# Kernel optimization log

Hardware: AMD Instinct MI355X
Metric: run time of the kernel (lower is better)

## Reference

```python
import jax, jax.numpy as jnp
import numpy as np

EPS = 1e-15


def setup_inputs() -> dict:
    key = jax.random.key(0)
    ks = jax.random.split(key, 10)
    F, B, L = 10, 16384, 20          # num_field, batch, hist_len
    V, D = 1000000, 16               # sparse_feature_number, sparse_feature_dim
    FEAT, E, S, G, T = 160, 8, 64, 3, 32  # feature_size, expert_num, expert_size, gate_num, tower_size
    return {
        "ids": jax.random.randint(ks[0], (F, B, L), 0, V, dtype=jnp.int64),
        "emb_table": jax.random.uniform(ks[1], (V, D), jnp.float32, -1.0, 1.0),
        "expert_w": jax.random.normal(ks[2], (E, FEAT, S), jnp.float32) * 0.05,
        "expert_b": jnp.full((E, S), 0.1, jnp.float32),
        "gate_w": jax.random.normal(ks[3], (G, FEAT, E), jnp.float32) * 0.05,
        "gate_b": jnp.full((G, E), 0.1, jnp.float32),
        "tower_w": jax.random.normal(ks[4], (G, S, T), jnp.float32) * 0.05,
        "tower_b": jnp.full((G, T), 0.1, jnp.float32),
        "out_w": jax.random.normal(ks[5], (G, T, 2), jnp.float32) * 0.05,
        "out_b": jnp.full((G, 2), 0.1, jnp.float32),
    }


def reference(ids, emb_table, expert_w, expert_b, gate_w, gate_b,
              tower_w, tower_b, out_w, out_b):
    # Embedding lookup + sum over history: [F,B,L,D] -> [F,B,D]
    field_emb = emb_table[ids].sum(axis=2)
    B = field_emb.shape[1]
    # concat per-field embeddings along feature axis: [B, F*D]
    x = jnp.transpose(field_emb, (1, 0, 2)).reshape(B, -1)
    # all experts as one batched GEMM: [B,E,S]
    experts = jax.nn.relu(jnp.einsum('bf,efs->bes', x, expert_w) + expert_b)
    # gate softmax over experts: [B,G,E]
    gates = jax.nn.softmax(jnp.einsum('bf,gfe->bge', x, gate_w) + gate_b, axis=-1)
    # gate-weighted expert mixture: [B,G,S]
    mix = jnp.einsum('bge,bes->bgs', gates, experts)
    # towers: [B,G,T] -> logits [B,G,2]
    tow = jax.nn.relu(jnp.einsum('bgs,gst->bgt', mix, tower_w) + tower_b)
    logits = jnp.einsum('bgt,gto->bgo', tow, out_w) + out_b
    probs = jnp.clip(jax.nn.softmax(logits, axis=-1), EPS, 1.0 - EPS)  # [B,3,2]
    ctr, cvr, imp = probs[:, 0], probs[:, 1], probs[:, 2]
    ctr1 = ctr[:, 1:2]
    cvr1 = cvr[:, 1:2]
    ctcvr1 = ctr1 * cvr1
    ctcvr = jnp.concatenate([1.0 - ctcvr1, ctcvr1], axis=1)
    imp1 = imp[:, 1:2]
    # out_list packed along last axis: ctr(2), ctr1(1), cvr(2), cvr1(1), ctcvr(2), ctcvr1(1), imp1(1) -> [B,10]
    return jnp.concatenate([ctr, ctr1, cvr, cvr1, ctcvr, ctcvr1, imp1], axis=1)
```

## Files before the change

kernel.cpp:

```cpp
#include <hip/hip_runtime.h>
#include <hip/hip_bf16.h>
#include <cstdint>
#include <cstddef>

#define NFIELD 10
#define BATCH  16384
#define NIDS   20
#define DEMB   16
#define NFEAT  160
#define NEXP   8
#define NS     64
#define NG     3
#define NT     32

#define XB        ((size_t)BATCH * NFEAT * 2)
#define BP_OFF_B  XB
#define BM_OFF_B  (BP_OFF_B + 174080)
#define BT_OFF_B  (BM_OFF_B + 2176)
#define TB2_OFF_B (BT_OFF_B + 12288)
#define OWF_OFF_B (TB2_OFF_B + 384)
#define OBF_OFF_B (OWF_OFF_B + 768)
#define FLG_OFF_B (OBF_OFF_B + 32)

typedef short bfrag __attribute__((ext_vector_type(8)));
typedef float f32x4 __attribute__((ext_vector_type(4)));

__device__ __forceinline__ float bflo(uint32_t u) {
    union { uint32_t u; float f; } c; c.u = u << 16; return c.f;
}
__device__ __forceinline__ float bfhi(uint32_t u) {
    union { uint32_t u; float f; } c; c.u = u & 0xffff0000u; return c.f;
}
__device__ __forceinline__ float bf1(uint16_t v) {
    union { uint32_t u; float f; } c; c.u = ((uint32_t)v) << 16; return c.f;
}
__device__ __forceinline__ uint16_t f2bf(float f) {
    union { float f; uint32_t u; } c; c.f = f;
    uint32_t r = c.u + 0x7fffu + ((c.u >> 16) & 1u);
    return (uint16_t)(r >> 16);
}
__device__ __forceinline__ float ldw(const void* p, int i, bool bf) {
    return bf ? bf1(((const uint16_t*)p)[i]) : ((const float*)p)[i];
}
__device__ __forceinline__ uint16_t ldb16(const void* p, int i, bool bf) {
    return bf ? ((const uint16_t*)p)[i] : f2bf(((const float*)p)[i]);
}

__global__ __launch_bounds__(64) void sniff_dtypes(
    const uint32_t* __restrict__ ids_w,
    const uint32_t* __restrict__ emb_w,
    int* __restrict__ flags)
{
    int t = threadIdx.x;
    size_t p = (size_t)t * 25000;
    uint32_t hi = ids_w[2 * p + 1];
    int n_hi = __popcll(__ballot(hi != 0));

    size_t q = (size_t)t * 125000;
    uint32_t w = emb_w[q];
    uint32_t v = (w >> 8) & 0x7Fu;
    int n_bf = __popcll(__ballot(v >= 0x3Bu && v <= 0x3Fu));

    if (t == 0) {
        flags[0] = (n_hi < 8)   ? 1 : 0;
        flags[1] = (n_bf >= 32) ? 1 : 0;
    }
}

__global__ __launch_bounds__(256) void pack_weights(
    const void* __restrict__ ew, const void* __restrict__ eb,
    const void* __restrict__ gw, const void* __restrict__ gb,
    const void* __restrict__ tw, const void* __restrict__ tb,
    const void* __restrict__ ow, const void* __restrict__ ob,
    uint16_t* __restrict__ bp, float* __restrict__ bm,
    uint16_t* __restrict__ bt, float* __restrict__ tb2,
    float* __restrict__ owf, float* __restrict__ obf,
    const int* __restrict__ flags)
{
    const bool bf = flags[1] != 0;
    int i = blockIdx.x * 256 + threadIdx.x;
    if (i < 10880) {
        int nt = i / 320, rem = i % 320;
        int ks = rem / 64, l = rem % 64;
        int n  = nt * 16 + (l & 15);
        int kb = ks * 32 + ((l >> 4) * 8);
        uint16_t v[8];
        #pragma unroll
        for (int j = 0; j < 8; ++j) {
            int k = kb + j;
            uint16_t x;
            if (n < 512)      x = ldb16(ew, (n >> 6) * 10240 + k * 64 + (n & 63), bf);
            else if (n < 536) x = ldb16(gw, ((n - 512) >> 3) * 1280 + k * 8 + ((n - 512) & 7), bf);
            else              x = 0;
            v[j] = x;
        }
        uint4 o;
        o.x = (uint32_t)v[0] | ((uint32_t)v[1] << 16);
        o.y = (uint32_t)v[2] | ((uint32_t)v[3] << 16);
        o.z = (uint32_t)v[4] | ((uint32_t)v[5] << 16);
        o.w = (uint32_t)v[6] | ((uint32_t)v[7] << 16);
        ((uint4*)bp)[i] = o;
    } else if (i < 11648) {
        int it = i - 10880;
        int g = it / 256, rem = it % 256;
        int ntile = rem / 128, ks = (rem / 64) & 1, l = rem % 64;
        int t  = ntile * 16 + (l & 15);
        int sb = ks * 32 + ((l >> 4) * 8);
        uint16_t v[8];
        #pragma unroll
        for (int j = 0; j < 8; ++j)
            v[j] = ldb16(tw, g * 2048 + (sb + j) * 32 + t, bf);
        uint4 o;
        o.x = (uint32_t)v[0] | ((uint32_t)v[1] << 16);
        o.y = (uint32_t)v[2] | ((uint32_t)v[3] << 16);
        o.z = (uint32_t)v[4] | ((uint32_t)v[5] << 16);
        o.w = (uint32_t)v[6] | ((uint32_t)v[7] << 16);
        ((uint4*)bt)[it] = o;
    } else if (i < 12192) {
        int n = i - 11648;
        bm[n] = (n < 512) ? ldw(eb, n, bf) : (n < 536 ? ldw(gb, n - 512, bf) : 0.0f);
    } else if (i < 12288) {
        int n = i - 12192; tb2[n] = ldw(tb, n, bf);
    } else if (i < 12480) {
        int n = i - 12288; owf[n] = ldw(ow, n, bf);
    } else if (i < 12486) {
        int n = i - 12480; obf[n] = ldw(ob, n, bf);
    }
}

__global__ __launch_bounds__(256) void gather_sum(
    const void* __restrict__ ids_raw,
    const void* __restrict__ emb_raw,
    uint16_t* __restrict__ xout,
    const int* __restrict__ flags)
{
    const bool i64 = flags[0] != 0;
    const bool bf  = flags[1] != 0;
    int tid = blockIdx.x * 256 + threadIdx.x;
    int h    = tid & 1;
    int pair = tid >> 1;
    int f = pair >> 14;
    int b = pair & (BATCH - 1);

    int idv[NIDS];
    if (i64) {
        const int4* p4 = (const int4*)((const long long*)ids_raw +
                                       ((size_t)f * BATCH + b) * NIDS);
        #pragma unroll
        for (int j = 0; j < NIDS / 2; ++j) {
            int4 q = p4[j];
            idv[2 * j + 0] = q.x;
            idv[2 * j + 1] = q.z;
        }
    } else {
        const int4* p4 = (const int4*)((const int*)ids_raw +
                                       ((size_t)f * BATCH + b) * NIDS);
        #pragma unroll
        for (int j = 0; j < NIDS / 4; ++j) {
            int4 q = p4[j];
            idv[4 * j + 0] = q.x; idv[4 * j + 1] = q.y;
            idv[4 * j + 2] = q.z; idv[4 * j + 3] = q.w;
        }
    }

    float acc[8];
    #pragma unroll
    for (int d = 0; d < 8; ++d) acc[d] = 0.0f;

    if (bf) {
        #pragma unroll
        for (int l = 0; l < NIDS; ++l) {
            uint4 r = *(const uint4*)((const uint16_t*)emb_raw +
                                      (size_t)idv[l] * DEMB + h * 8);
            acc[0] += bflo(r.x); acc[1] += bfhi(r.x);
            acc[2] += bflo(r.y); acc[3] += bfhi(r.y);
            acc[4] += bflo(r.z); acc[5] += bfhi(r.z);
            acc[6] += bflo(r.w); acc[7] += bfhi(r.w);
        }
    } else {
        #pragma unroll
        for (int l = 0; l < NIDS; ++l) {
            const float4* p = (const float4*)((const float*)emb_raw +
                                              (size_t)idv[l] * DEMB + h * 8);
            float4 r0 = p[0], r1 = p[1];
            acc[0] += r0.x; acc[1] += r0.y; acc[2] += r0.z; acc[3] += r0.w;
            acc[4] += r1.x; acc[5] += r1.y; acc[6] += r1.z; acc[7] += r1.w;
        }
    }

    uint4 o;
    o.x = (uint32_t)f2bf(acc[0]) | ((uint32_t)f2bf(acc[1]) << 16);
    o.y = (uint32_t)f2bf(acc[2]) | ((uint32_t)f2bf(acc[3]) << 16);
    o.z = (uint32_t)f2bf(acc[4]) | ((uint32_t)f2bf(acc[5]) << 16);
    o.w = (uint32_t)f2bf(acc[6]) | ((uint32_t)f2bf(acc[7]) << 16);
    *(uint4*)(xout + (size_t)b * NFEAT + f * DEMB + h * 8) = o;
}

__global__ __launch_bounds__(256) void moe_fwd(
    const uint16_t* __restrict__ xbf,
    const uint16_t* __restrict__ bp,
    const float*    __restrict__ bm,
    const uint16_t* __restrict__ btw,
    const float*    __restrict__ btb,
    const float*    __restrict__ owf,
    const float*    __restrict__ obf,
    const int* __restrict__ flags,
    void* __restrict__ out)
{
    __shared__ uint16_t exp_lds[32][520];
    __shared__ float    gate_lds[32][33];
    __shared__ uint16_t mix_lds[32][200];
    __shared__ float    tow_lds[32][100];
    __shared__ float    prob_lds[32][6];

    const bool bfw = flags[1] != 0;
    const int tid = threadIdx.x;
    const int w = tid >> 6, l = tid & 63;
    const int lm = l & 15, q = l >> 4;
    const int b0 = blockIdx.x * 32;
    const int mrow = (w & 1) * 16;
    const int nhalf = w >> 1;

    bfrag a[5];
    {
        const uint16_t* xr = xbf + (size_t)(b0 + mrow + lm) * NFEAT + q * 8;
        #pragma unroll
        for (int ks = 0; ks < 5; ++ks)
            a[ks] = *(const bfrag*)(xr + ks * 32);
    }

    const int nt0 = nhalf * 17;
    for (int it = 0; it < 17; ++it) {
        int nt = nt0 + it;
        f32x4 acc = {0.0f, 0.0f, 0.0f, 0.0f};
        const bfrag* bpp = (const bfrag*)bp + (size_t)(nt * 5) * 64 + l;
        #pragma unroll
        for (int ks = 0; ks < 5; ++ks) {
            bfrag b = bpp[ks * 64];
            acc = __builtin_amdgcn_mfma_f32_16x16x32_bf16(a[ks], b, acc, 0, 0, 0);
        }
        int col = nt * 16 + lm;
        float bias = bm[col];
        if (col < 512) {
            #pragma unroll
            for (int r = 0; r < 4; ++r)
                exp_lds[mrow + q * 4 + r][col] = f2bf(fmaxf(acc[r] + bias, 0.0f));
        } else {
            #pragma unroll
            for (int r = 0; r < 4; ++r)
                gate_lds[mrow + q * 4 + r][col - 512] = acc[r] + bias;
        }
    }
    __syncthreads();

    const int sm = tid >> 3, j = tid & 7;

    if (j < 3) {
        float* gl = &gate_lds[sm][j * 8];
        float m = gl[0];
        #pragma unroll
        for (int e = 1; e < 8; ++e) m = fmaxf(m, gl[e]);
        float ex[8], s = 0.0f;
        #pragma unroll
        for (int e = 0; e < 8; ++e) { ex[e] = __expf(gl[e] - m); s += ex[e]; }
        float inv = 1.0f / s;
        #pragma unroll
        for (int e = 0; e < 8; ++e) gl[e] = ex[e] * inv;
    }
    __syncthreads();

    for (int g = 0; g < NG; ++g) {
        float m8[8];
        #pragma unroll
        for (int i = 0; i < 8; ++i) m8[i] = 0.0f;
        #pragma unroll
        for (int e = 0; e < NEXP; ++e) {
            float gv = gate_lds[sm][g * 8 + e];
            uint4 u = *(const uint4*)&exp_lds[sm][e * 64 + j * 8];
            m8[0] = fmaf(gv, bflo(u.x), m8[0]); m8[1] = fmaf(gv, bfhi(u.x), m8[1]);
            m8[2] = fmaf(gv, bflo(u.y), m8[2]); m8[3] = fmaf(gv, bfhi(u.y), m8[3]);
            m8[4] = fmaf(gv, bflo(u.z), m8[4]); m8[5] = fmaf(gv, bfhi(u.z), m8[5]);
            m8[6] = fmaf(gv, bflo(u.w), m8[6]); m8[7] = fmaf(gv, bfhi(u.w), m8[7]);
        }
        uint4 o;
        o.x = (uint32_t)f2bf(m8[0]) | ((uint32_t)f2bf(m8[1]) << 16);
        o.y = (uint32_t)f2bf(m8[2]) | ((uint32_t)f2bf(m8[3]) << 16);
        o.z = (uint32_t)f2bf(m8[4]) | ((uint32_t)f2bf(m8[5]) << 16);
        o.w = (uint32_t)f2bf(m8[6]) | ((uint32_t)f2bf(m8[7]) << 16);
        *(uint4*)&mix_lds[sm][g * 64 + j * 8] = o;
    }
    __syncthreads();

    for (int u = w; u < 12; u += 4) {
        int g = u >> 2, mt = (u >> 1) & 1, ntile = u & 1;
        f32x4 acc = {0.0f, 0.0f, 0.0f, 0.0f};
        #pragma unroll
        for (int ks = 0; ks < 2; ++ks) {
            bfrag av = *(const bfrag*)&mix_lds[mt * 16 + lm][g * 64 + ks * 32 + q * 8];
            bfrag bv = *(const bfrag*)(btw + (size_t)((((g * 2 + ntile) * 2 + ks) * 64 + l)) * 8);
            acc = __builtin_amdgcn_mfma_f32_16x16x32_bf16(av, bv, acc, 0, 0, 0);
        }
        int t = ntile * 16 + lm;
        float bias = btb[g * 32 + t];
        #pragma unroll
        for (int r = 0; r < 4; ++r)
            tow_lds[mt * 16 + q * 4 + r][g * 32 + t] = fmaxf(acc[r] + bias, 0.0f);
    }
    __syncthreads();

    if (j < 3) {
        int g = j;
        float l0 = obf[2 * g], l1 = obf[2 * g + 1];
        #pragma unroll 8
        for (int t = 0; t < NT; ++t) {
            float tv = tow_lds[sm][g * 32 + t];
            l0 = fmaf(tv, owf[g * 64 + 2 * t], l0);
            l1 = fmaf(tv, owf[g * 64 + 2 * t + 1], l1);
        }
        float m  = fmaxf(l0, l1);
        float e0 = __expf(l0 - m);
        float e1 = __expf(l1 - m);
        float inv = 1.0f / (e0 + e1);
        float p0 = fminf(fmaxf(e0 * inv, 1e-15f), 1.0f);
        float p1 = fminf(fmaxf(e1 * inv, 1e-15f), 1.0f);
        prob_lds[sm][2 * g + 0] = p0;
        prob_lds[sm][2 * g + 1] = p1;
    }
    __syncthreads();

    {
        float ctr0 = prob_lds[sm][0], ctr1 = prob_lds[sm][1];
        float cvr0 = prob_lds[sm][2], cvr1 = prob_lds[sm][3];
        float imp1 = prob_lds[sm][5];
        float ctcvr1 = ctr1 * cvr1;
        for (int o = j; o < 10; o += 8) {
            float v;
            switch (o) {
                case 0: v = ctr0; break;
                case 1: v = ctr1; break;
                case 2: v = ctr1; break;
                case 3: v = cvr0; break;
                case 4: v = cvr1; break;
                case 5: v = cvr1; break;
                case 6: v = 1.0f - ctcvr1; break;
                case 7: v = ctcvr1; break;
                case 8: v = ctcvr1; break;
                default: v = imp1; break;
            }
            if (bfw) ((uint16_t*)out)[(size_t)(b0 + sm) * 10 + o] = f2bf(v);
            else     ((float*)out)[(size_t)(b0 + sm) * 10 + o]    = v;
        }
    }
}

extern "C" void kernel_launch(void* const* d_in, const int* in_sizes, int n_in,
                              void* d_out, int out_size, void* d_ws, size_t ws_size,
                              hipStream_t stream) {
    const void* ids = d_in[0];
    const void* emb = d_in[1];

    char* ws = (char*)d_ws;
    uint16_t* xbf = (uint16_t*)ws;
    uint16_t* bpk = (uint16_t*)(ws + BP_OFF_B);
    float*    bm  = (float*)(ws + BM_OFF_B);
    uint16_t* btw = (uint16_t*)(ws + BT_OFF_B);
    float*    tb2 = (float*)(ws + TB2_OFF_B);
    float*    owf = (float*)(ws + OWF_OFF_B);
    float*    obf = (float*)(ws + OBF_OFF_B);
    int*    flags = (int*)(ws + FLG_OFF_B);

    sniff_dtypes<<<1, 64, 0, stream>>>((const uint32_t*)ids, (const uint32_t*)emb, flags);
    pack_weights<<<49, 256, 0, stream>>>(
        d_in[2], d_in[3], d_in[4], d_in[5], d_in[6], d_in[7], d_in[8], d_in[9],
        bpk, bm, btw, tb2, owf, obf, flags);
    gather_sum<<<(NFIELD * BATCH * 2) / 256, 256, 0, stream>>>(ids, emb, xbf, flags);
    moe_fwd<<<BATCH / 32, 256, 0, stream>>>(
        xbf, bpk, bm, btw, tb2, owf, obf, flags, d_out);
}
```

Before: 204.9 us.

## Fuse embedding gather into MoE kernel and inline dtype sniffing

Removes the separate gather_sum and sniff_dtypes kernels. Each MoE block now gathers and sums embeddings for its 32 rows directly into shared memory, one thread per (field,row) covering all 16 dims. Dtype detection moves into per-block inline sniffing. This avoids the global round trip of the bf16 feature matrix and two launches, but leaves fewer threads issuing the random gathers and serialises gather before the MFMA phase within each block.

Measured after the change: 177.0 us. 1.16x faster.

```diff
diff --git a/kernel.cpp b/kernel.cpp
--- a/kernel.cpp
+++ b/kernel.cpp
@@ -13,14 +13,12 @@
 #define NG     3
 #define NT     32
 
-#define XB        ((size_t)BATCH * NFEAT * 2)
-#define BP_OFF_B  XB
+#define BP_OFF_B  0
 #define BM_OFF_B  (BP_OFF_B + 174080)
 #define BT_OFF_B  (BM_OFF_B + 2176)
 #define TB2_OFF_B (BT_OFF_B + 12288)
 #define OWF_OFF_B (TB2_OFF_B + 384)
 #define OBF_OFF_B (OWF_OFF_B + 768)
-#define FLG_OFF_B (OBF_OFF_B + 32)
 
 typedef short bfrag __attribute__((ext_vector_type(8)));
 typedef float f32x4 __attribute__((ext_vector_type(4)));
@@ -45,39 +43,32 @@
 __device__ __forceinline__ uint16_t ldb16(const void* p, int i, bool bf) {
     return bf ? ((const uint16_t*)p)[i] : f2bf(((const float*)p)[i]);
 }
-
-__global__ __launch_bounds__(64) void sniff_dtypes(
-    const uint32_t* __restrict__ ids_w,
+__device__ __forceinline__ int sniff_bf(const uint32_t* emb_w) {
+    int n_bf = 0;
+    #pragma unroll
+    for (int t = 0; t < 16; ++t) {
+        uint32_t wv = emb_w[(size_t)t * 500000];
+        uint32_t v = (wv >> 8) & 0x7Fu;
+        n_bf += (v >= 0x3Bu && v <= 0x3Fu);
+    }
+    return n_bf >= 8;
+}
+
+__global__ __launch_bounds__(256) void pack_weights(
     const uint32_t* __restrict__ emb_w,
-    int* __restrict__ flags)
-{
-    int t = threadIdx.x;
-    size_t p = (size_t)t * 25000;
-    uint32_t hi = ids_w[2 * p + 1];
-    int n_hi = __popcll(__ballot(hi != 0));
-
-    size_t q = (size_t)t * 125000;
-    uint32_t w = emb_w[q];
-    uint32_t v = (w >> 8) & 0x7Fu;
-    int n_bf = __popcll(__ballot(v >= 0x3Bu && v <= 0x3Fu));
-
-    if (t == 0) {
-        flags[0] = (n_hi < 8)   ? 1 : 0;
-        flags[1] = (n_bf >= 32) ? 1 : 0;
-    }
-}
-
-__global__ __launch_bounds__(256) void pack_weights(
     const void* __restrict__ ew, const void* __restrict__ eb,
     const void* __restrict__ gw, const void* __restrict__ gb,
     const void* __restrict__ tw, const void* __restrict__ tb,
     const void* __restrict__ ow, const void* __restrict__ ob,
     uint16_t* __restrict__ bp, float* __restrict__ bm,
     uint16_t* __restrict__ bt, float* __restrict__ tb2,
-    float* __restrict__ owf, float* __restrict__ obf,
-    const int* __restrict__ flags)
+    float* __restrict__ owf, float* __restrict__ obf)
 {
-    const bool bf = flags[1] != 0;
+    __shared__ int sbf;
+    if (threadIdx.x == 0) sbf = sniff_bf(emb_w);
+    __syncthreads();
+    const bool bf = sbf != 0;
+
     int i = blockIdx.x * 256 + threadIdx.x;
     if (i < 10880) {
         int nt = i / 320, rem = i % 320;
@@ -128,83 +119,15 @@
     }
 }
 
-__global__ __launch_bounds__(256) void gather_sum(
+__global__ __launch_bounds__(256, 2) void moe_fused(
     const void* __restrict__ ids_raw,
     const void* __restrict__ emb_raw,
-    uint16_t* __restrict__ xout,
-    const int* __restrict__ flags)
-{
-    const bool i64 = flags[0] != 0;
-    const bool bf  = flags[1] != 0;
-    int tid = blockIdx.x * 256 + threadIdx.x;
-    int h    = tid & 1;
-    int pair = tid >> 1;
-    int f = pair >> 14;
-    int b = pair & (BATCH - 1);
-
-    int idv[NIDS];
-    if (i64) {
-        const int4* p4 = (const int4*)((const long long*)ids_raw +
-                                       ((size_t)f * BATCH + b) * NIDS);
-        #pragma unroll
-        for (int j = 0; j < NIDS / 2; ++j) {
-            int4 q = p4[j];
-            idv[2 * j + 0] = q.x;
-            idv[2 * j + 1] = q.z;
-        }
-    } else {
-        const int4* p4 = (const int4*)((const int*)ids_raw +
-                                       ((size_t)f * BATCH + b) * NIDS);
-        #pragma unroll
-        for (int j = 0; j < NIDS / 4; ++j) {
-            int4 q = p4[j];
-            idv[4 * j + 0] = q.x; idv[4 * j + 1] = q.y;
-            idv[4 * j + 2] = q.z; idv[4 * j + 3] = q.w;
-        }
-    }
-
-    float acc[8];
-    #pragma unroll
-    for (int d = 0; d < 8; ++d) acc[d] = 0.0f;
-
-    if (bf) {
-        #pragma unroll
-        for (int l = 0; l < NIDS; ++l) {
-            uint4 r = *(const uint4*)((const uint16_t*)emb_raw +
-                                      (size_t)idv[l] * DEMB + h * 8);
-            acc[0] += bflo(r.x); acc[1] += bfhi(r.x);
-            acc[2] += bflo(r.y); acc[3] += bfhi(r.y);
-            acc[4] += bflo(r.z); acc[5] += bfhi(r.z);
-            acc[6] += bflo(r.w); acc[7] += bfhi(r.w);
-        }
-    } else {
-        #pragma unroll
-        for (int l = 0; l < NIDS; ++l) {
-            const float4* p = (const float4*)((const float*)emb_raw +
-                                              (size_t)idv[l] * DEMB + h * 8);
-            float4 r0 = p[0], r1 = p[1];
-            acc[0] += r0.x; acc[1] += r0.y; acc[2] += r0.z; acc[3] += r0.w;
-            acc[4] += r1.x; acc[5] += r1.y; acc[6] += r1.z; acc[7] += r1.w;
-        }
-    }
-
-    uint4 o;
-    o.x = (uint32_t)f2bf(acc[0]) | ((uint32_t)f2bf(acc[1]) << 16);
-    o.y = (uint32_t)f2bf(acc[2]) | ((uint32_t)f2bf(acc[3]) << 16);
-    o.z = (uint32_t)f2bf(acc[4]) | ((uint32_t)f2bf(acc[5]) << 16);
-    o.w = (uint32_t)f2bf(acc[6]) | ((uint32_t)f2bf(acc[7]) << 16);
-    *(uint4*)(xout + (size_t)b * NFEAT + f * DEMB + h * 8) = o;
-}
-
-__global__ __launch_bounds__(256) void moe_fwd(
-    const uint16_t* __restrict__ xbf,
     const uint16_t* __restrict__ bp,
     const float*    __restrict__ bm,
     const uint16_t* __restrict__ btw,
     const float*    __restrict__ btb,
     const float*    __restrict__ owf,
     const float*    __restrict__ obf,
-    const int* __restrict__ flags,
     void* __restrict__ out)
 {
     __shared__ uint16_t exp_lds[32][520];
@@ -212,8 +135,8 @@
     __shared__ uint16_t mix_lds[32][200];
     __shared__ float    tow_lds[32][100];
     __shared__ float    prob_lds[32][6];
-
-    const bool bfw = flags[1] != 0;
+    __shared__ int      sflags;
+
     const int tid = threadIdx.x;
     const int w = tid >> 6, l = tid & 63;
     const int lm = l & 15, q = l >> 4;
@@ -221,13 +144,91 @@
     const int mrow = (w & 1) * 16;
     const int nhalf = w >> 1;
 
+    if (tid == 0) {
+        int n_hi = 0;
+        #pragma unroll
+        for (int t = 0; t < 16; ++t) {
+            size_t p = (size_t)t * 100000;
+            n_hi += (((const uint32_t*)ids_raw)[2 * p + 1] != 0);
+        }
+        sflags = ((n_hi < 2) ? 1 : 0) | (sniff_bf((const uint32_t*)emb_raw) ? 2 : 0);
+    }
+    __syncthreads();
+    const bool i64 = (sflags & 1) != 0;
+    const bool bfe = (sflags & 2) != 0;
+
+    uint16_t* xs = &exp_lds[0][0];
+    for (int p = tid; p < 32 * NFIELD; p += 256) {
+        int f = p >> 5, s = p & 31;
+        int idv[NIDS];
+        if (i64) {
+            const int4* p4 = (const int4*)((const long long*)ids_raw +
+                                           ((size_t)f * BATCH + (b0 + s)) * NIDS);
+            #pragma unroll
+            for (int j = 0; j < NIDS / 2; ++j) {
+                int4 t4 = p4[j];
+                idv[2 * j + 0] = t4.x;
+                idv[2 * j + 1] = t4.z;
+            }
+        } else {
+            const int4* p4 = (const int4*)((const int*)ids_raw +
+                                           ((size_t)f * BATCH + (b0 + s)) * NIDS);
+            #pragma unroll
+            for (int j = 0; j < NIDS / 4; ++j) {
+                int4 t4 = p4[j];
+                idv[4 * j + 0] = t4.x; idv[4 * j + 1] = t4.y;
+                idv[4 * j + 2] = t4.z; idv[4 * j + 3] = t4.w;
+            }
+        }
+
+        float acc[16];
+        #pragma unroll
+        for (int d = 0; d < 16; ++d) acc[d] = 0.0f;
+
+        if (bfe) {
+            #pragma unroll 5
+            for (int ll = 0; ll < NIDS; ++ll) {
+                const uint4* row = (const uint4*)((const uint16_t*)emb_raw +
+                                                  (size_t)idv[ll] * DEMB);
+                uint4 r0 = row[0];
+                uint4 r1 = row[1];
+                acc[0]  += bflo(r0.x); acc[1]  += bfhi(r0.x);
+                acc[2]  += bflo(r0.y); acc[3]  += bfhi(r0.y);
+                acc[4]  += bflo(r0.z); acc[5]  += bfhi(r0.z);
+                acc[6]  += bflo(r0.w); acc[7]  += bfhi(r0.w);
+                acc[8]  += bflo(r1.x); acc[9]  += bfhi(r1.x);
+                acc[10] += bflo(r1.y); acc[11] += bfhi(r1.y);
+                acc[12] += bflo(r1.z); acc[13] += bfhi(r1.z);
+                acc[14] += bflo(r1.w); acc[15] += bfhi(r1.w);
+            }
+        } else {
+            #pragma unroll 5
+            for (int ll = 0; ll < NIDS; ++ll) {
+                const float4* row = (const float4*)((const float*)emb_raw +
+                                                    (size_t)idv[ll] * DEMB);
+                float4 r0 = row[0], r1 = row[1], r2 = row[2], r3 = row[3];
+                acc[0]  += r0.x; acc[1]  += r0.y; acc[2]  += r0.z; acc[3]  += r0.w;
+                acc[4]  += r1.x; acc[5]  += r1.y; acc[6]  += r1.z; acc[7]  += r1.w;
+                acc[8]  += r2.x; acc[9]  += r2.y; acc[10] += r2.z; acc[11] += r2.w;
+                acc[12] += r3.x; acc[13] += r3.y; acc[14] += r3.z; acc[15] += r3.w;
+            }
+        }
+
+        uint32_t pk[8];
+        #pragma unroll
+        for (int j = 0; j < 8; ++j)
+            pk[j] = (uint32_t)f2bf(acc[2 * j]) | ((uint32_t)f2bf(acc[2 * j + 1]) << 16);
+        uint4* dst = (uint4*)(xs + (size_t)s * 168 + f * DEMB);
+        dst[0] = make_uint4(pk[0], pk[1], pk[2], pk[3]);
+        dst[1] = make_uint4(pk[4], pk[5], pk[6], pk[7]);
+    }
+    __syncthreads();
+
     bfrag a[5];
-    {
-        const uint16_t* xr = xbf + (size_t)(b0 + mrow + lm) * NFEAT + q * 8;
-        #pragma unroll
-        for (int ks = 0; ks < 5; ++ks)
-            a[ks] = *(const bfrag*)(xr + ks * 32);
-    }
+    #pragma unroll
+    for (int ks = 0; ks < 5; ++ks)
+        a[ks] = *(const bfrag*)(xs + (size_t)(mrow + lm) * 168 + ks * 32 + q * 8);
+    __syncthreads();
 
     const int nt0 = nhalf * 17;
     for (int it = 0; it < 17; ++it) {
@@ -347,7 +348,7 @@
                 case 8: v = ctcvr1; break;
                 default: v = imp1; break;
             }
-            if (bfw) ((uint16_t*)out)[(size_t)(b0 + sm) * 10 + o] = f2bf(v);
+            if (bfe) ((uint16_t*)out)[(size_t)(b0 + sm) * 10 + o] = f2bf(v);
             else     ((float*)out)[(size_t)(b0 + sm) * 10 + o]    = v;
         }
     }
@@ -360,20 +361,17 @@
     const void* emb = d_in[1];
 
     char* ws = (char*)d_ws;
-    uint16_t* xbf = (uint16_t*)ws;
     uint16_t* bpk = (uint16_t*)(ws + BP_OFF_B);
     float*    bm  = (float*)(ws + BM_OFF_B);
     uint16_t* btw = (uint16_t*)(ws + BT_OFF_B);
     float*    tb2 = (float*)(ws + TB2_OFF_B);
     float*    owf = (float*)(ws + OWF_OFF_B);
     float*    obf = (float*)(ws + OBF_OFF_B);
-    int*    flags = (int*)(ws + FLG_OFF_B);
-
-    sniff_dtypes<<<1, 64, 0, stream>>>((const uint32_t*)ids, (const uint32_t*)emb, flags);
+
     pack_weights<<<49, 256, 0, stream>>>(
+        (const uint32_t*)emb,
         d_in[2], d_in[3], d_in[4], d_in[5], d_in[6], d_in[7], d_in[8], d_in[9],
-        bpk, bm, btw, tb2, owf, obf, flags);
-    gather_sum<<<(NFIELD * BATCH * 2) / 256, 256, 0, stream>>>(ids, emb, xbf, flags);
-    moe_fwd<<<BATCH / 32, 256, 0, stream>>>(
-        xbf, bpk, bm, btw, tb2, owf, obf, flags, d_out);
-}
+        bpk, bm, btw, tb2, owf, obf);
+    moe_fused<<<BATCH / 32, 256, 0, stream>>>(
+        ids, emb, bpk, bm, btw, tb2, owf, obf, d_out);
+}
```
